# Performance work log

Hardware: AMD Instinct MI355X
Metric: run time of the kernel (lower is better)

The kernel has to match this reference:

```python
import jax, jax.numpy as jnp
import numpy as np

T_SCALE = 10.0   # self.t = ones(1)*10
EPS = 1e-8       # torch cosine_similarity eps


def setup_inputs() -> dict:
    key = jax.random.key(0)
    k1, k2, k3 = jax.random.split(key, 3)
    B, D, C = 2048, 25088, 100
    feature = jax.random.normal(k1, (B, D), dtype=jnp.float32)
    label = jax.random.randint(k2, (B,), 0, C, dtype=jnp.int64)
    # mimic reset_parameters: uniform(-stdv, stdv), stdv = 1/sqrt(in_dim)
    stdv = 1.0 / np.sqrt(D)
    weight = jax.random.uniform(k3, (C, D), dtype=jnp.float32, minval=-stdv, maxval=stdv)
    return {"feature": feature, "label": label, "weight": weight}


def _cos_logits(feature, weight):
    # Equivalent to t * cosine_similarity over broadcasted (B, C, D):
    # L2-normalize rows (with torch's eps clamp on norms) then matmul.
    fn = feature / jnp.maximum(jnp.linalg.norm(feature, axis=-1, keepdims=True), EPS)
    wn = weight / jnp.maximum(jnp.linalg.norm(weight, axis=-1, keepdims=True), EPS)
    return T_SCALE * jnp.einsum('bd,cd->bc', fn, wn)  # [B, C]


def reference(feature, label, weight):
    pred = _cos_logits(feature, weight)                      # [B, C]
    logp = jax.nn.log_softmax(pred, axis=-1)
    valid = (label >= 0)
    safe_label = jnp.where(valid, label, 0)
    nll = -jnp.take_along_axis(logp, safe_label[:, None], axis=1)[:, 0]
    vmask = valid.astype(pred.dtype)
    n_valid = jnp.sum(vmask)
    loss = jnp.sum(nll * vmask) / jnp.maximum(n_valid, 1.0)  # CE with ignore_index=-1
    preds = jnp.argmax(pred, axis=1)
    acc = jnp.sum(vmask * (preds == label).astype(pred.dtype)) / (n_valid + 1e-10)
    return loss, acc
```

## Files before the change

kernel.cpp:

```cpp
#include <hip/hip_runtime.h>
#include <hip/hip_bf16.h>

#define D_DIM   25088
#define B_ROWS  2048
#define C_CLS   100
#define NT      7
#define NPAD    112
#define KSTEPS_TOTAL 784
#define SPLITS  56
#define KSTEPS_PER (KSTEPS_TOTAL / SPLITS)
#define EPS     1e-8f

typedef __bf16 bf16x8 __attribute__((ext_vector_type(8)));
typedef float  f32x4  __attribute__((ext_vector_type(4)));
typedef float  f32x2  __attribute__((ext_vector_type(2)));

__device__ __forceinline__ unsigned bfpack2(float lo, float hi) {
    unsigned a = __builtin_bit_cast(unsigned, lo);
    unsigned b = __builtin_bit_cast(unsigned, hi);
    a += 0x7FFFu + ((a >> 16) & 1u);
    b += 0x7FFFu + ((b >> 16) & 1u);
    return (a >> 16) | (b & 0xFFFF0000u);
}

__global__ __launch_bounds__(256) void prep_kernel(const float* __restrict__ w,
                                                   float* __restrict__ wscale,
                                                   unsigned* __restrict__ wpack) {
    int c = blockIdx.x;
    int t = c >> 4, n = c & 15;
    bool real = (c < C_CLS);
    const float* row = w + (size_t)c * D_DIM;
    float s = 0.f;
    for (int i = 0; i < 49; ++i) {
        int d = i * 512 + threadIdx.x * 2;
        f32x2 v = {0.f, 0.f};
        if (real) v = *(const f32x2*)(row + d);
        s += v[0]*v[0] + v[1]*v[1];
        int gstep = d >> 5, r = d & 31, quad = r >> 3, j = r & 7;
        unsigned dw = bfpack2(v[0], v[1]);
        size_t idx = ((size_t)(gstep * 7 + t) * 64 + quad * 16 + n) * 4 + (j >> 1);
        wpack[idx] = dw;
    }
    if (!real) return;
    __shared__ float red[4];
    for (int o = 32; o; o >>= 1) s += __shfl_down(s, o, 64);
    if ((threadIdx.x & 63) == 0) red[threadIdx.x >> 6] = s;
    __syncthreads();
    if (threadIdx.x == 0) {
        float nn = sqrtf(red[0] + red[1] + red[2] + red[3]);
        wscale[c] = 1.0f / fmaxf(nn, EPS);
    }
}

__global__ __launch_bounds__(256, 4) void gemm_kernel(const float* __restrict__ feat,
                                                      const uint4* __restrict__ wpack,
                                                      float* __restrict__ pred,
                                                      float* __restrict__ fnorm2) {
    int tid  = threadIdx.x;
    int wave = tid >> 6, lane = tid & 63;
    int m = lane & 15, quad = lane >> 4;
    int rowbase = blockIdx.x * 64 + wave * 16;
    int row = rowbase + m;
    int gstep0 = blockIdx.y * KSTEPS_PER;

    const float* pA = feat + (size_t)row * D_DIM + gstep0 * 32 + quad * 8;
    const uint4* pB = wpack + (size_t)gstep0 * NT * 64 + lane;

    f32x4 acc[NT];
#pragma unroll
    for (int t = 0; t < NT; ++t) acc[t] = (f32x4){0.f,0.f,0.f,0.f};
    float sumsq = 0.f;

    f32x4 a0 = *(const f32x4*)(pA);
    f32x4 a1 = *(const f32x4*)(pA + 4);

    for (int s = 0; s < KSTEPS_PER; ++s) {
        const float* pn = pA + ((s + 1 < KSTEPS_PER) ? 32 : 0);
        f32x4 n0 = *(const f32x4*)(pn);
        f32x4 n1 = *(const f32x4*)(pn + 4);

        sumsq += a0[0]*a0[0] + a0[1]*a0[1] + a0[2]*a0[2] + a0[3]*a0[3]
               + a1[0]*a1[0] + a1[1]*a1[1] + a1[2]*a1[2] + a1[3]*a1[3];
        uint4 ap;
        ap.x = bfpack2(a0[0], a0[1]);
        ap.y = bfpack2(a0[2], a0[3]);
        ap.z = bfpack2(a1[0], a1[1]);
        ap.w = bfpack2(a1[2], a1[3]);
        bf16x8 afrag = __builtin_bit_cast(bf16x8, ap);
#pragma unroll
        for (int t = 0; t < NT; ++t) {
            bf16x8 bfrag = __builtin_bit_cast(bf16x8, pB[t * 64]);
            acc[t] = __builtin_amdgcn_mfma_f32_16x16x32_bf16(afrag, bfrag, acc[t], 0, 0, 0);
        }
        a0 = n0; a1 = n1;
        pA += 32;
        pB += NT * 64;
    }

    sumsq += __shfl_xor(sumsq, 16, 64);
    sumsq += __shfl_xor(sumsq, 32, 64);
    if (quad == 0) atomicAdd(&fnorm2[row], sumsq);

#pragma unroll
    for (int t = 0; t < NT; ++t) {
#pragma unroll
        for (int r = 0; r < 4; ++r) {
            int orow = rowbase + quad * 4 + r;
            int ocol = t * 16 + m;
            atomicAdd(&pred[(size_t)orow * NPAD + ocol], acc[t][r]);
        }
    }
}

__global__ __launch_bounds__(256) void finalize_kernel(const float* __restrict__ pred,
                                                       const float* __restrict__ fnorm2,
                                                       const float* __restrict__ wscale,
                                                       const int* __restrict__ label,
                                                       float* __restrict__ scal) {
    int gwave = (blockIdx.x * 256 + threadIdx.x) >> 6;
    int lane = threadIdx.x & 63;
    int row = gwave;
    if (row >= B_ROWS) return;
    float finv = 10.0f / fmaxf(sqrtf(fnorm2[row]), EPS);
    const float* pr = pred + (size_t)row * NPAD;

    int c0 = lane, c1 = lane + 64;
    float l0 = (c0 < C_CLS) ? pr[c0] * wscale[c0] * finv : -1e30f;
    float l1 = (c1 < C_CLS) ? pr[c1] * wscale[c1] * finv : -1e30f;

    float mx = l0; int am = c0;
    if (l1 > mx) { mx = l1; am = c1; }
    for (int o = 1; o < 64; o <<= 1) {
        float om = __shfl_xor(mx, o, 64);
        int   oa = __shfl_xor(am, o, 64);
        if (om > mx || (om == mx && oa < am)) { mx = om; am = oa; }
    }
    float se = expf(l0 - mx) + expf(l1 - mx);
    for (int o = 1; o < 64; o <<= 1) se += __shfl_xor(se, o, 64);

    int lab = label[row];
    int labc = (lab < 0) ? 0 : lab;
    float lv = (labc >= 64) ? l1 : l0;
    float ll = __shfl(lv, labc & 63, 64);

    if (lane == 0 && lab >= 0) {
        float lse = mx + logf(se);
        atomicAdd(&scal[0], lse - ll);
        atomicAdd(&scal[1], (am == lab) ? 1.f : 0.f);
        atomicAdd(&scal[2], 1.f);
    }
}

__global__ void out_kernel(const float* __restrict__ scal, float* __restrict__ out) {
    out[0] = scal[0] / fmaxf(scal[2], 1.0f);
    out[1] = scal[1] / (scal[2] + 1e-10f);
}

extern "C" void kernel_launch(void* const* d_in, const int* in_sizes, int n_in,
                              void* d_out, int out_size, void* d_ws, size_t ws_size,
                              hipStream_t stream) {
    const float* feat   = (const float*)d_in[0];
    const int*   label  = (const int*)d_in[1];
    const float* weight = (const float*)d_in[2];
    float* out = (float*)d_out;

    char* ws = (char*)d_ws;
    float* pred   = (float*)(ws);
    float* fnorm2 = (float*)(ws + 917504);
    float* scal   = (float*)(ws + 925696);
    float* wscale = (float*)(ws + 925712);
    uint4* wpack  = (uint4*)(ws + 926720);

    hipMemsetAsync(ws, 0, 925712, stream);
    prep_kernel<<<NPAD, 256, 0, stream>>>(weight, wscale, (unsigned*)wpack);
    gemm_kernel<<<dim3(B_ROWS / 64, SPLITS), 256, 0, stream>>>(feat, wpack, pred, fnorm2);
    finalize_kernel<<<B_ROWS / 4 / 64, 256, 0, stream>>>(pred, fnorm2, wscale, label, scal);
    out_kernel<<<1, 1, 0, stream>>>(scal, out);
}
```

Before: 366.2 us.

## Split weight prep across blocks, raise GEMM occupancy, fix finalize grid and labels

The weight prep kernel is split across 7 blocks per class along D. Each block atomically accumulates its partial squared norm, and finalize computes the inverse norm, so prep gets more parallelism on a mostly idle device. The GEMM launch bound is raised to 8 waves-per-EU blocks, which may cap registers and cause spills. The finalize grid previously covered only 32 rows and now covers all 2048, and int64 labels are read correctly. Both of those are correctness fixes that add a little work.

```diff
diff --git a/kernel.cpp b/kernel.cpp
--- a/kernel.cpp
+++ b/kernel.cpp
@@ -24,15 +24,17 @@
 }
 
 __global__ __launch_bounds__(256) void prep_kernel(const float* __restrict__ w,
-                                                   float* __restrict__ wscale,
+                                                   float* __restrict__ wnorm2,
                                                    unsigned* __restrict__ wpack) {
     int c = blockIdx.x;
     int t = c >> 4, n = c & 15;
     bool real = (c < C_CLS);
     const float* row = w + (size_t)c * D_DIM;
     float s = 0.f;
-    for (int i = 0; i < 49; ++i) {
-        int d = i * 512 + threadIdx.x * 2;
+    int i0 = blockIdx.y * 7;
+#pragma unroll
+    for (int ii = 0; ii < 7; ++ii) {
+        int d = (i0 + ii) * 512 + threadIdx.x * 2;
         f32x2 v = {0.f, 0.f};
         if (real) v = *(const f32x2*)(row + d);
         s += v[0]*v[0] + v[1]*v[1];
@@ -46,13 +48,10 @@
     for (int o = 32; o; o >>= 1) s += __shfl_down(s, o, 64);
     if ((threadIdx.x & 63) == 0) red[threadIdx.x >> 6] = s;
     __syncthreads();
-    if (threadIdx.x == 0) {
-        float nn = sqrtf(red[0] + red[1] + red[2] + red[3]);
-        wscale[c] = 1.0f / fmaxf(nn, EPS);
-    }
+    if (threadIdx.x == 0) atomicAdd(&wnorm2[c], red[0] + red[1] + red[2] + red[3]);
 }
 
-__global__ __launch_bounds__(256, 4) void gemm_kernel(const float* __restrict__ feat,
+__global__ __launch_bounds__(256, 8) void gemm_kernel(const float* __restrict__ feat,
                                                       const uint4* __restrict__ wpack,
                                                       float* __restrict__ pred,
                                                       float* __restrict__ fnorm2) {
@@ -114,8 +113,9 @@
 
 __global__ __launch_bounds__(256) void finalize_kernel(const float* __restrict__ pred,
                                                        const float* __restrict__ fnorm2,
-                                                       const float* __restrict__ wscale,
-                                                       const int* __restrict__ label,
+                                                       const float* __restrict__ wnorm2,
+                                                       const void* __restrict__ labp,
+                                                       int lab64,
                                                        float* __restrict__ scal) {
     int gwave = (blockIdx.x * 256 + threadIdx.x) >> 6;
     int lane = threadIdx.x & 63;
@@ -125,8 +125,15 @@
     const float* pr = pred + (size_t)row * NPAD;
 
     int c0 = lane, c1 = lane + 64;
-    float l0 = (c0 < C_CLS) ? pr[c0] * wscale[c0] * finv : -1e30f;
-    float l1 = (c1 < C_CLS) ? pr[c1] * wscale[c1] * finv : -1e30f;
+    float l0 = -1e30f, l1 = -1e30f;
+    if (c0 < C_CLS) {
+        float ws = 1.0f / fmaxf(sqrtf(wnorm2[c0]), EPS);
+        l0 = pr[c0] * ws * finv;
+    }
+    if (c1 < C_CLS) {
+        float ws = 1.0f / fmaxf(sqrtf(wnorm2[c1]), EPS);
+        l1 = pr[c1] * ws * finv;
+    }
 
     float mx = l0; int am = c0;
     if (l1 > mx) { mx = l1; am = c1; }
@@ -138,7 +145,7 @@
     float se = expf(l0 - mx) + expf(l1 - mx);
     for (int o = 1; o < 64; o <<= 1) se += __shfl_xor(se, o, 64);
 
-    int lab = label[row];
+    int lab = lab64 ? (int)((const long long*)labp)[row] : ((const int*)labp)[row];
     int labc = (lab < 0) ? 0 : lab;
     float lv = (labc >= 64) ? l1 : l0;
     float ll = __shfl(lv, labc & 63, 64);
@@ -160,7 +167,7 @@
                               void* d_out, int out_size, void* d_ws, size_t ws_size,
                               hipStream_t stream) {
     const float* feat   = (const float*)d_in[0];
-    const int*   label  = (const int*)d_in[1];
+    const void*  label  = d_in[1];
     const float* weight = (const float*)d_in[2];
     float* out = (float*)d_out;
 
@@ -168,12 +175,14 @@
     float* pred   = (float*)(ws);
     float* fnorm2 = (float*)(ws + 917504);
     float* scal   = (float*)(ws + 925696);
-    float* wscale = (float*)(ws + 925712);
+    float* wnorm2 = (float*)(ws + 925712);
     uint4* wpack  = (uint4*)(ws + 926720);
 
-    hipMemsetAsync(ws, 0, 925712, stream);
-    prep_kernel<<<NPAD, 256, 0, stream>>>(weight, wscale, (unsigned*)wpack);
+    int lab64 = (n_in > 1 && in_sizes[1] >= B_ROWS * 8) ? 1 : 0;
+
+    hipMemsetAsync(ws, 0, 926160, stream);
+    prep_kernel<<<dim3(NPAD, 7), 256, 0, stream>>>(weight, wnorm2, (unsigned*)wpack);
     gemm_kernel<<<dim3(B_ROWS / 64, SPLITS), 256, 0, stream>>>(feat, wpack, pred, fnorm2);
-    finalize_kernel<<<B_ROWS / 4 / 64, 256, 0, stream>>>(pred, fnorm2, wscale, label, scal);
+    finalize_kernel<<<B_ROWS / 4, 256, 0, stream>>>(pred, fnorm2, wnorm2, label, lab64, scal);
     out_kernel<<<1, 1, 0, stream>>>(scal, out);
 }
```

After: 425.3 us. 1.16x slower.
